# Kernel tuning notes

Hardware: AMD Instinct MI355X
Metric: run time of the kernel (lower is better)

## Reference

```python
import jax, jax.numpy as jnp
import numpy as np

N, NFEAT = 8192, 128

def _unif(k, shape, fan_out):
    s = 1.0 / np.sqrt(fan_out)
    return jax.random.uniform(k, shape, jnp.float32, -s, s)

def setup_inputs() -> dict:
    key = jax.random.key(0)
    ks = jax.random.split(key, 10)
    x = jax.random.normal(ks[0], (N, NFEAT), jnp.float32)
    adj = jax.random.uniform(ks[1], (N, N), jnp.float32)  # all > 0 -> full degree
    W1 = _unif(ks[2], (NFEAT, 10), 10); b1 = _unif(ks[3], (10,), 10)
    W2 = _unif(ks[4], (10, 5), 5);      b2 = _unif(ks[5], (5,), 5)
    fc1_W = _unif(ks[6], (5, 5), 5);    fc1_b = _unif(ks[7], (5,), 5)
    fc_W = _unif(ks[8], (5, 2), 2);     fc_b = _unif(ks[9], (2,), 2)
    return dict(x=x, adj=adj, W1=W1, b1=b1, W2=W2, b2=b2,
                fc1_W=fc1_W, fc1_b=fc1_b, fc_W=fc_W, fc_b=fc_b)

def _gcn(x, adj, W, b):
    # D = diag(row-wise count of adj > 0); A_tilda = D^-1/2 (A + I) D^-1/2
    deg = jnp.sum((adj > 0.0).astype(x.dtype), axis=1)
    dinv = deg ** -0.5                       # [N]
    s = (x @ W) * dinv[:, None]              # D^-1/2 @ (X W), [N, out]
    out = dinv[:, None] * (adj @ s + s)      # D^-1/2 @ (A + I) @ s
    return out + b

def reference(x, adj, W1, b1, W2, b2, fc1_W, fc1_b, fc_W, fc_b):
    h = jax.nn.relu(_gcn(x, adj, W1, b1))    # [N, 10]
    h = _gcn(h, adj, W2, b2)                 # [N, 5]
    z = jax.nn.relu(jnp.mean(h, axis=0))     # [5]
    z2 = jax.nn.relu(z @ fc1_W + fc1_b)      # [5]
    y = jax.nn.sigmoid(z2 @ fc_W + fc_b)     # [2]
    return (z, y)
```

## Files before the change

kernel.cpp:

```cpp
#include <hip/hip_runtime.h>
#include <math.h>

#define NN 8192
#define NF 128


__global__ __launch_bounds__(256) void kA(const float* __restrict__ adj,
                                          float* __restrict__ dinv,
                                          float* __restrict__ c0,
                                          int* __restrict__ Zcount,
                                          int* __restrict__ Zlist) {
    const int t = threadIdx.x;
    const int lane = t & 63, wid = t >> 6;
    const int rowBase = blockIdx.x * 32;
    float4 csum[8];
#pragma unroll
    for (int q = 0; q < 8; q++) csum[q] = make_float4(0.f, 0.f, 0.f, 0.f);
    __shared__ int wsum[4];

    for (int r = 0; r < 32; r++) {
        const int i = rowBase + r;
        const float4* arow = (const float4*)(adj + (size_t)i * NN);
        int cnt = 0;
#pragma unroll
        for (int it = 0; it < 8; it++) {
            float4 a = arow[it * 256 + t];
            csum[it].x += a.x; csum[it].y += a.y;
            csum[it].z += a.z; csum[it].w += a.w;
            cnt += (a.x > 0.f) + (a.y > 0.f) + (a.z > 0.f) + (a.w > 0.f);
        }
#pragma unroll
        for (int off = 32; off > 0; off >>= 1) cnt += __shfl_xor(cnt, off, 64);
        if (lane == 0) wsum[wid] = cnt;
        __syncthreads();
        if (t == 0) {
            int d = wsum[0] + wsum[1] + wsum[2] + wsum[3];
            dinv[i] = rsqrtf((float)d);
            if (d != NN) { int p = atomicAdd(Zcount, 1); Zlist[p] = i; }
        }
        __syncthreads();
    }
#pragma unroll
    for (int it = 0; it < 8; it++) {
        int j = (it * 256 + t) * 4;
        atomicAdd(&c0[j + 0], csum[it].x);
        atomicAdd(&c0[j + 1], csum[it].y);
        atomicAdd(&c0[j + 2], csum[it].z);
        atomicAdd(&c0[j + 3], csum[it].w);
    }
}

__global__ __launch_bounds__(256) void kC(const float* __restrict__ adj,
                                          const float* __restrict__ dinv,
                                          float* __restrict__ c0,
                                          const int* __restrict__ Zcount,
                                          const int* __restrict__ Zlist) {
    int j = blockIdx.x * 256 + threadIdx.x;
    const float dinv0 = rsqrtf((float)NN);
    float v = c0[j] * dinv0;
    int zc = *Zcount;
    for (int p = 0; p < zc; p++) {
        int zi = Zlist[p];
        v += (dinv[zi] - dinv0) * adj[(size_t)zi * NN + j];
    }
    c0[j] = v;
}

__global__ __launch_bounds__(256) void kS1(const float* __restrict__ x,
                                           const float* __restrict__ W1,
                                           const float* __restrict__ dinv,
                                           float* __restrict__ s1) {
    __shared__ float sW[NF * 10];
    for (int i = threadIdx.x; i < NF * 10; i += 256) sW[i] = W1[i];
    __syncthreads();
    int tid = blockIdx.x * 256 + threadIdx.x;
    int j = tid / 10, k = tid % 10;
    const float4* xr = (const float4*)(x + (size_t)j * NF);
    float s = 0.f;
#pragma unroll
    for (int f4 = 0; f4 < 32; f4++) {
        float4 a = xr[f4];
        s += a.x * sW[(f4 * 4 + 0) * 10 + k] + a.y * sW[(f4 * 4 + 1) * 10 + k]
           + a.z * sW[(f4 * 4 + 2) * 10 + k] + a.w * sW[(f4 * 4 + 3) * 10 + k];
    }
    s1[tid] = s * dinv[j];
}

__global__ __launch_bounds__(256) void kP(const float* __restrict__ adj,
                                          const float* __restrict__ s1,
                                          const float* __restrict__ dinv,
                                          const float* __restrict__ b1,
                                          float* __restrict__ h) {
    const int t = threadIdx.x;
    const int lane = t & 63, wid = t >> 6;
    const int i0 = blockIdx.x * 16 + wid * 4;
    float acc[4][10];
#pragma unroll
    for (int r = 0; r < 4; r++)
#pragma unroll
        for (int k = 0; k < 10; k++) acc[r][k] = 0.f;

    const float4* a0p = (const float4*)(adj + (size_t)(i0 + 0) * NN);
    const float4* a1p = (const float4*)(adj + (size_t)(i0 + 1) * NN);
    const float4* a2p = (const float4*)(adj + (size_t)(i0 + 2) * NN);
    const float4* a3p = (const float4*)(adj + (size_t)(i0 + 3) * NN);

    for (int it = 0; it < 32; it++) {
        int vi = it * 64 + lane;
        float4 a0 = a0p[vi], a1 = a1p[vi], a2 = a2p[vi], a3 = a3p[vi];
        const float4* sp = (const float4*)(s1 + (size_t)vi * 40);
        float sv[40];
#pragma unroll
        for (int q = 0; q < 10; q++) {
            float4 v = sp[q];
            sv[q * 4 + 0] = v.x; sv[q * 4 + 1] = v.y;
            sv[q * 4 + 2] = v.z; sv[q * 4 + 3] = v.w;
        }
#pragma unroll
        for (int k = 0; k < 10; k++) {
            acc[0][k] += a0.x * sv[k] + a0.y * sv[10 + k] + a0.z * sv[20 + k] + a0.w * sv[30 + k];
            acc[1][k] += a1.x * sv[k] + a1.y * sv[10 + k] + a1.z * sv[20 + k] + a1.w * sv[30 + k];
            acc[2][k] += a2.x * sv[k] + a2.y * sv[10 + k] + a2.z * sv[20 + k] + a2.w * sv[30 + k];
            acc[3][k] += a3.x * sv[k] + a3.y * sv[10 + k] + a3.z * sv[20 + k] + a3.w * sv[30 + k];
        }
    }
#pragma unroll
    for (int r = 0; r < 4; r++)
#pragma unroll
        for (int k = 0; k < 10; k++)
#pragma unroll
            for (int off = 32; off > 0; off >>= 1)
                acc[r][k] += __shfl_xor(acc[r][k], off, 64);

    if (lane == 0) {
#pragma unroll
        for (int r = 0; r < 4; r++) {
            int i = i0 + r;
            float di = dinv[i];
#pragma unroll
            for (int k = 0; k < 10; k++) {
                float v = di * (acc[r][k] + s1[i * 10 + k]) + b1[k];
                h[i * 10 + k] = fmaxf(v, 0.f);
            }
        }
    }
}

__global__ __launch_bounds__(256) void kF1(const float* __restrict__ h,
                                           const float* __restrict__ dinv,
                                           const float* __restrict__ c0,
                                           const float* __restrict__ W2,
                                           float* __restrict__ accum) {
    int j = blockIdx.x * 256 + threadIdx.x;
    float hv[10];
#pragma unroll
    for (int m = 0; m < 10; m++) hv[m] = h[j * 10 + m];
    float dj = dinv[j], cj = c0[j];
    float p[10];
#pragma unroll
    for (int k = 0; k < 5; k++) {
        float s = 0.f;
#pragma unroll
        for (int m = 0; m < 10; m++) s += hv[m] * W2[m * 5 + k];
        s *= dj;
        p[k] = cj * s;
        p[5 + k] = dj * s;
    }
#pragma unroll
    for (int q = 0; q < 10; q++) {
        float v = p[q];
#pragma unroll
        for (int off = 32; off > 0; off >>= 1) v += __shfl_xor(v, off, 64);
        if ((threadIdx.x & 63) == 0) atomicAdd(&accum[q], v);
    }
}

__global__ void kF2(const float* __restrict__ accum, const float* __restrict__ b2,
                    const float* __restrict__ fc1W, const float* __restrict__ fc1b,
                    const float* __restrict__ fcW, const float* __restrict__ fcb,
                    float* __restrict__ out) {
    if (threadIdx.x == 0 && blockIdx.x == 0) {
        float z[5];
        for (int k = 0; k < 5; k++) {
            float v = (accum[k] + accum[5 + k]) * (1.f / (float)NN) + b2[k];
            z[k] = fmaxf(v, 0.f);
            out[k] = z[k];
        }
        float z2[5];
        for (int m = 0; m < 5; m++) {
            float v = fc1b[m];
            for (int k = 0; k < 5; k++) v += z[k] * fc1W[k * 5 + m];
            z2[m] = fmaxf(v, 0.f);
        }
        for (int n = 0; n < 2; n++) {
            float v = fcb[n];
            for (int m = 0; m < 5; m++) v += z2[m] * fcW[m * 2 + n];
            out[5 + n] = 1.f / (1.f + expf(-v));
        }
    }
}

extern "C" void kernel_launch(void* const* d_in, const int* in_sizes, int n_in,
                              void* d_out, int out_size, void* d_ws, size_t ws_size,
                              hipStream_t stream) {
    const float* x    = (const float*)d_in[0];
    const float* adj  = (const float*)d_in[1];
    const float* W1   = (const float*)d_in[2];
    const float* b1   = (const float*)d_in[3];
    const float* W2   = (const float*)d_in[4];
    const float* b2   = (const float*)d_in[5];
    const float* fc1W = (const float*)d_in[6];
    const float* fc1b = (const float*)d_in[7];
    const float* fcW  = (const float*)d_in[8];
    const float* fcb  = (const float*)d_in[9];
    (void)in_sizes; (void)n_in; (void)out_size; (void)ws_size;

    float* ws    = (float*)d_ws;
    float* dinv  = ws;
    float* c0    = ws + 8192;
    float* s1    = ws + 16384;
    float* h     = ws + 98304;
    float* accum = ws + 180224;
    int*   Zcount = (int*)(ws + 180240);
    int*   Zlist  = (int*)(ws + 180244);
    float* out = (float*)d_out;

    hipMemsetAsync(c0, 0, 8192 * sizeof(float), stream);
    hipMemsetAsync(accum, 0, 20 * sizeof(float), stream);

    kA <<<256, 256, 0, stream>>>(adj, dinv, c0, Zcount, Zlist);
    kC <<<32,  256, 0, stream>>>(adj, dinv, c0, Zcount, Zlist);
    kS1<<<320, 256, 0, stream>>>(x, W1, dinv, s1);
    kP <<<512, 256, 0, stream>>>(adj, s1, dinv, b1, h);
    kF1<<<32,  256, 0, stream>>>(h, dinv, c0, W2, accum);
    kF2<<<1,   64,  0, stream>>>(accum, b2, fc1W, fc1b, fcW, fcb, out);
}
```

Baseline: 520.4 us.

## Fuse degree/column-sum pass into adjacency SpMM with deferred degree correction

```diff
diff --git a/kernel.cpp b/kernel.cpp
--- a/kernel.cpp
+++ b/kernel.cpp
@@ -5,71 +5,9 @@
 #define NF 128
 
 
-__global__ __launch_bounds__(256) void kA(const float* __restrict__ adj,
-                                          float* __restrict__ dinv,
-                                          float* __restrict__ c0,
-                                          int* __restrict__ Zcount,
-                                          int* __restrict__ Zlist) {
-    const int t = threadIdx.x;
-    const int lane = t & 63, wid = t >> 6;
-    const int rowBase = blockIdx.x * 32;
-    float4 csum[8];
-#pragma unroll
-    for (int q = 0; q < 8; q++) csum[q] = make_float4(0.f, 0.f, 0.f, 0.f);
-    __shared__ int wsum[4];
-
-    for (int r = 0; r < 32; r++) {
-        const int i = rowBase + r;
-        const float4* arow = (const float4*)(adj + (size_t)i * NN);
-        int cnt = 0;
-#pragma unroll
-        for (int it = 0; it < 8; it++) {
-            float4 a = arow[it * 256 + t];
-            csum[it].x += a.x; csum[it].y += a.y;
-            csum[it].z += a.z; csum[it].w += a.w;
-            cnt += (a.x > 0.f) + (a.y > 0.f) + (a.z > 0.f) + (a.w > 0.f);
-        }
-#pragma unroll
-        for (int off = 32; off > 0; off >>= 1) cnt += __shfl_xor(cnt, off, 64);
-        if (lane == 0) wsum[wid] = cnt;
-        __syncthreads();
-        if (t == 0) {
-            int d = wsum[0] + wsum[1] + wsum[2] + wsum[3];
-            dinv[i] = rsqrtf((float)d);
-            if (d != NN) { int p = atomicAdd(Zcount, 1); Zlist[p] = i; }
-        }
-        __syncthreads();
-    }
-#pragma unroll
-    for (int it = 0; it < 8; it++) {
-        int j = (it * 256 + t) * 4;
-        atomicAdd(&c0[j + 0], csum[it].x);
-        atomicAdd(&c0[j + 1], csum[it].y);
-        atomicAdd(&c0[j + 2], csum[it].z);
-        atomicAdd(&c0[j + 3], csum[it].w);
-    }
-}
-
-__global__ __launch_bounds__(256) void kC(const float* __restrict__ adj,
-                                          const float* __restrict__ dinv,
-                                          float* __restrict__ c0,
-                                          const int* __restrict__ Zcount,
-                                          const int* __restrict__ Zlist) {
-    int j = blockIdx.x * 256 + threadIdx.x;
-    const float dinv0 = rsqrtf((float)NN);
-    float v = c0[j] * dinv0;
-    int zc = *Zcount;
-    for (int p = 0; p < zc; p++) {
-        int zi = Zlist[p];
-        v += (dinv[zi] - dinv0) * adj[(size_t)zi * NN + j];
-    }
-    c0[j] = v;
-}
-
-__global__ __launch_bounds__(256) void kS1(const float* __restrict__ x,
-                                           const float* __restrict__ W1,
-                                           const float* __restrict__ dinv,
-                                           float* __restrict__ s1) {
+__global__ __launch_bounds__(256) void kS1p(const float* __restrict__ x,
+                                            const float* __restrict__ W1,
+                                            float* __restrict__ s1p) {
     __shared__ float sW[NF * 10];
     for (int i = threadIdx.x; i < NF * 10; i += 256) sW[i] = W1[i];
     __syncthreads();
@@ -83,22 +21,29 @@
         s += a.x * sW[(f4 * 4 + 0) * 10 + k] + a.y * sW[(f4 * 4 + 1) * 10 + k]
            + a.z * sW[(f4 * 4 + 2) * 10 + k] + a.w * sW[(f4 * 4 + 3) * 10 + k];
     }
-    s1[tid] = s * dinv[j];
-}
-
-__global__ __launch_bounds__(256) void kP(const float* __restrict__ adj,
-                                          const float* __restrict__ s1,
-                                          const float* __restrict__ dinv,
-                                          const float* __restrict__ b1,
-                                          float* __restrict__ h) {
+    s1p[tid] = s;
+}
+
+__global__ __launch_bounds__(512) void kFuse(const float* __restrict__ adj,
+                                             const float* __restrict__ s1p,
+                                             float* __restrict__ accO,
+                                             float* __restrict__ dinv,
+                                             float* __restrict__ c0,
+                                             int* __restrict__ Zcount,
+                                             int* __restrict__ Zlist) {
+    __shared__ float lcs[4][2048];
     const int t = threadIdx.x;
     const int lane = t & 63, wid = t >> 6;
-    const int i0 = blockIdx.x * 16 + wid * 4;
+    for (int n = t; n < 8192; n += 512) ((float*)lcs)[n] = 0.f;
+    __syncthreads();
+
+    const int i0 = blockIdx.x * 32 + wid * 4;
     float acc[4][10];
 #pragma unroll
     for (int r = 0; r < 4; r++)
 #pragma unroll
         for (int k = 0; k < 10; k++) acc[r][k] = 0.f;
+    int cnt[4] = {0, 0, 0, 0};
 
     const float4* a0p = (const float4*)(adj + (size_t)(i0 + 0) * NN);
     const float4* a1p = (const float4*)(adj + (size_t)(i0 + 1) * NN);
@@ -106,9 +51,9 @@
     const float4* a3p = (const float4*)(adj + (size_t)(i0 + 3) * NN);
 
     for (int it = 0; it < 32; it++) {
-        int vi = it * 64 + lane;
+        const int vi = it * 64 + lane;
         float4 a0 = a0p[vi], a1 = a1p[vi], a2 = a2p[vi], a3 = a3p[vi];
-        const float4* sp = (const float4*)(s1 + (size_t)vi * 40);
+        const float4* sp = (const float4*)(s1p + (size_t)vi * 40);
         float sv[40];
 #pragma unroll
         for (int q = 0; q < 10; q++) {
@@ -123,52 +68,88 @@
             acc[2][k] += a2.x * sv[k] + a2.y * sv[10 + k] + a2.z * sv[20 + k] + a2.w * sv[30 + k];
             acc[3][k] += a3.x * sv[k] + a3.y * sv[10 + k] + a3.z * sv[20 + k] + a3.w * sv[30 + k];
         }
-    }
-#pragma unroll
-    for (int r = 0; r < 4; r++)
+        atomicAdd(&lcs[0][vi], a0.x + a1.x + a2.x + a3.x);
+        atomicAdd(&lcs[1][vi], a0.y + a1.y + a2.y + a3.y);
+        atomicAdd(&lcs[2][vi], a0.z + a1.z + a2.z + a3.z);
+        atomicAdd(&lcs[3][vi], a0.w + a1.w + a2.w + a3.w);
+        cnt[0] += (a0.x > 0.f) + (a0.y > 0.f) + (a0.z > 0.f) + (a0.w > 0.f);
+        cnt[1] += (a1.x > 0.f) + (a1.y > 0.f) + (a1.z > 0.f) + (a1.w > 0.f);
+        cnt[2] += (a2.x > 0.f) + (a2.y > 0.f) + (a2.z > 0.f) + (a2.w > 0.f);
+        cnt[3] += (a3.x > 0.f) + (a3.y > 0.f) + (a3.z > 0.f) + (a3.w > 0.f);
+    }
+
+#pragma unroll
+    for (int r = 0; r < 4; r++) {
 #pragma unroll
         for (int k = 0; k < 10; k++)
 #pragma unroll
             for (int off = 32; off > 0; off >>= 1)
                 acc[r][k] += __shfl_xor(acc[r][k], off, 64);
+#pragma unroll
+        for (int off = 32; off > 0; off >>= 1)
+            cnt[r] += __shfl_xor(cnt[r], off, 64);
+    }
 
     if (lane == 0) {
 #pragma unroll
         for (int r = 0; r < 4; r++) {
-            int i = i0 + r;
-            float di = dinv[i];
-#pragma unroll
-            for (int k = 0; k < 10; k++) {
-                float v = di * (acc[r][k] + s1[i * 10 + k]) + b1[k];
-                h[i * 10 + k] = fmaxf(v, 0.f);
-            }
-        }
-    }
-}
-
-__global__ __launch_bounds__(256) void kF1(const float* __restrict__ h,
-                                           const float* __restrict__ dinv,
-                                           const float* __restrict__ c0,
-                                           const float* __restrict__ W2,
-                                           float* __restrict__ accum) {
-    int j = blockIdx.x * 256 + threadIdx.x;
+            const int i = i0 + r;
+            dinv[i] = rsqrtf((float)cnt[r]);
+            if (cnt[r] != NN) { int p = atomicAdd(Zcount, 1); Zlist[p] = i; }
+#pragma unroll
+            for (int k = 0; k < 10; k++) accO[i * 10 + k] = acc[r][k];
+        }
+    }
+
+    __syncthreads();
+    for (int n = t; n < 8192; n += 512)
+        atomicAdd(&c0[n], lcs[n & 3][n >> 2]);
+}
+
+__global__ __launch_bounds__(256) void kTail(const float* __restrict__ adj,
+                                             const float* __restrict__ accI,
+                                             const float* __restrict__ s1p,
+                                             const float* __restrict__ dinv,
+                                             const float* __restrict__ c0,
+                                             const int* __restrict__ Zcount,
+                                             const int* __restrict__ Zlist,
+                                             const float* __restrict__ b1,
+                                             const float* __restrict__ W2,
+                                             float* __restrict__ accum) {
+    const int j = blockIdx.x * 256 + threadIdx.x;
+    const float dinv0 = rsqrtf((float)NN);
+    const float dj = dinv[j];
+    float cj = c0[j] * dinv0;
     float hv[10];
 #pragma unroll
-    for (int m = 0; m < 10; m++) hv[m] = h[j * 10 + m];
-    float dj = dinv[j], cj = c0[j];
-    float p[10];
+    for (int k = 0; k < 10; k++) hv[k] = dinv0 * accI[j * 10 + k];
+
+    const int zc = *Zcount;
+    for (int p = 0; p < zc; p++) {
+        const int zi = Zlist[p];
+        const float dz = dinv[zi] - dinv0;
+        cj += dz * adj[(size_t)zi * NN + j];
+        const float az = dz * adj[(size_t)j * NN + zi];
+#pragma unroll
+        for (int k = 0; k < 10; k++) hv[k] += az * s1p[zi * 10 + k];
+    }
+#pragma unroll
+    for (int k = 0; k < 10; k++)
+        hv[k] = fmaxf(dj * (hv[k] + dj * s1p[j * 10 + k]) + b1[k], 0.f);
+
+    float p10[10];
 #pragma unroll
     for (int k = 0; k < 5; k++) {
         float s = 0.f;
 #pragma unroll
         for (int m = 0; m < 10; m++) s += hv[m] * W2[m * 5 + k];
         s *= dj;
-        p[k] = cj * s;
-        p[5 + k] = dj * s;
+        p10[k] = cj * s;
+        p10[5 + k] = dj * s;
     }
 #pragma unroll
     for (int q = 0; q < 10; q++) {
-        float v = p[q];
+        float v = p10[q];
 #pragma unroll
         for (int off = 32; off > 0; off >>= 1) v += __shfl_xor(v, off, 64);
         if ((threadIdx.x & 63) == 0) atomicAdd(&accum[q], v);
@@ -218,8 +199,8 @@
     float* ws    = (float*)d_ws;
     float* dinv  = ws;
     float* c0    = ws + 8192;
-    float* s1    = ws + 16384;
-    float* h     = ws + 98304;
+    float* s1p   = ws + 16384;
+    float* acc   = ws + 98304;
     float* accum = ws + 180224;
     int*   Zcount = (int*)(ws + 180240);
     int*   Zlist  = (int*)(ws + 180244);
@@ -228,10 +209,8 @@
     hipMemsetAsync(c0, 0, 8192 * sizeof(float), stream);
     hipMemsetAsync(accum, 0, 20 * sizeof(float), stream);
 
-    kA <<<256, 256, 0, stream>>>(adj, dinv, c0, Zcount, Zlist);
-    kC <<<32,  256, 0, stream>>>(adj, dinv, c0, Zcount, Zlist);
-    kS1<<<320, 256, 0, stream>>>(x, W1, dinv, s1);
-    kP <<<512, 256, 0, stream>>>(adj, s1, dinv, b1, h);
-    kF1<<<32,  256, 0, stream>>>(h, dinv, c0, W2, accum);
-    kF2<<<1,   64,  0, stream>>>(accum, b2, fc1W, fc1b, fcW, fcb, out);
-}
+    kS1p <<<320, 256, 0, stream>>>(x, W1, s1p);
+    kFuse<<<256, 512, 0, stream>>>(adj, s1p, acc, dinv, c0, Zcount, Zlist);
+    kTail<<<32,  256, 0, stream>>>(adj, acc, s1p, dinv, c0, Zcount, Zlist, b1, W2, accum);
+    kF2  <<<1,   64,  0, stream>>>(accum, b2, fc1W, fc1b, fcW, fcb, out);
+}
```

New measurement: 466.0 us. 10.4% less time.
